# Kernel optimization log

Hardware: AMD Instinct MI355X
Metric: run time of the kernel (lower is better)

## Reference

```python
import jax, jax.numpy as jnp
import numpy as np

N_CLASS = 20          # foreground classes (VOC)
SCORE_THR = 0.05
NMS_THR = 0.3
IMG_H, IMG_W = 600, 800
R = 2000              # number of proposed ROIs


def setup_inputs() -> dict:
    key = jax.random.key(0)
    k1, k2, k3, k4, k5 = jax.random.split(key, 5)
    # well-formed proposal boxes (y1, x1, y2, x2)
    cy = jax.random.uniform(k1, (R,), minval=0.0, maxval=float(IMG_H))
    cx = jax.random.uniform(k2, (R,), minval=0.0, maxval=float(IMG_W))
    hw = jax.random.uniform(k3, (R, 2), minval=20.0, maxval=200.0)
    h, w = hw[:, 0], hw[:, 1]
    boxes = jnp.stack([
        jnp.clip(cy - 0.5 * h, 0.0, IMG_H),
        jnp.clip(cx - 0.5 * w, 0.0, IMG_W),
        jnp.clip(cy + 0.5 * h, 0.0, IMG_H),
        jnp.clip(cx + 0.5 * w, 0.0, IMG_W),
    ], axis=1).astype(jnp.float32)
    loc = (0.2 * jax.random.normal(k4, (R, 4 * (N_CLASS + 1)))).astype(jnp.float32)
    score = (2.0 * jax.random.normal(k5, (R, N_CLASS + 1))).astype(jnp.float32)
    return {
        "proposed_roi_bboxes": boxes,
        "predicted_roi_loc": loc,
        "predicted_roi_score": score,
        "img_height": IMG_H,
        "img_width": IMG_W,
    }


def _pairwise_iou(b):
    # b: [N, 4] in (y1, x1, y2, x2); IoU is invariant to axis order
    tl = jnp.maximum(b[:, None, :2], b[None, :, :2])
    br = jnp.minimum(b[:, None, 2:], b[None, :, 2:])
    wh = jnp.clip(br - tl, 0.0)
    inter = wh[..., 0] * wh[..., 1]
    area = (b[:, 2] - b[:, 0]) * (b[:, 3] - b[:, 1])
    union = area[:, None] + area[None, :] - inter
    return inter / jnp.maximum(union, 1e-9)


def _nms_keep(boxes_sorted, valid_sorted, thr):
    # boxes sorted by descending score; returns keep mask [N]
    N = boxes_sorted.shape[0]
    iou = _pairwise_iou(boxes_sorted)          # [N, N]
    idx = jnp.arange(N)
    def body(suppressed, i):
        keep_i = valid_sorted[i] & (~suppressed[i])
        suppressed = suppressed | (keep_i & (iou[i] > thr) & (idx > i))
        return suppressed, keep_i
    _, keep = jax.lax.scan(body, jnp.zeros((N,), bool), idx)
    return keep


def _detect(proposed_roi_bboxes, predicted_roi_loc, predicted_roi_score, H, W):
    Rn = proposed_roi_bboxes.shape[0]
    C1 = N_CLASS + 1
    b = proposed_roi_bboxes
    loc = predicted_roi_loc.reshape(Rn, C1, 4)
    # Utility.loc2bbox (y1,x1,y2,x2 <-> cy,cx,h,w)
    src_h = b[:, 2] - b[:, 0]
    src_w = b[:, 3] - b[:, 1]
    src_cy = b[:, 0] + 0.5 * src_h
    src_cx = b[:, 1] + 0.5 * src_w
    dy, dx, dh, dw = loc[..., 0], loc[..., 1], loc[..., 2], loc[..., 3]
    cy = dy * src_h[:, None] + src_cy[:, None]
    cx = dx * src_w[:, None] + src_cx[:, None]
    hh = jnp.exp(dh) * src_h[:, None]
    ww = jnp.exp(dw) * src_w[:, None]
    boxes = jnp.stack([cy - 0.5 * hh, cx - 0.5 * ww,
                       cy + 0.5 * hh, cx + 0.5 * ww], axis=-1)  # [R, C1, 4]
    # clamp: even coords (y) to [0,H], odd coords (x) to [0,W]
    boxes = jnp.stack([
        jnp.clip(boxes[..., 0], 0.0, H),
        jnp.clip(boxes[..., 1], 0.0, W),
        jnp.clip(boxes[..., 2], 0.0, H),
        jnp.clip(boxes[..., 3], 0.0, W),
    ], axis=-1)
    prob = jax.nn.softmax(predicted_roi_score, axis=1)          # [R, C1]

    # foreground classes 1..N_CLASS -> leading class axis [C, R, ...]
    fg_boxes = jnp.transpose(boxes[:, 1:, :], (1, 0, 2))        # [C, R, 4]
    fg_prob = prob[:, 1:].T                                     # [C, R]
    valid = fg_prob > SCORE_THR
    sort_key = jnp.where(valid, fg_prob, -jnp.inf)
    order = jnp.argsort(-sort_key, axis=1)                      # [C, R]
    boxes_s = jnp.take_along_axis(fg_boxes, order[..., None], axis=1)
    prob_s = jnp.take_along_axis(fg_prob, order, axis=1)
    valid_s = jnp.take_along_axis(valid, order, axis=1)

    keep = jax.vmap(_nms_keep, in_axes=(0, 0, None))(boxes_s, valid_s, NMS_THR)  # [C, R] bool

    km = keep.astype(boxes_s.dtype)
    out = jnp.concatenate([boxes_s, prob_s[..., None]], axis=-1) * km[..., None]  # [C, R, 5]
    labels = jnp.arange(1, N_CLASS + 1, dtype=boxes_s.dtype)[:, None] * km        # [C, R]
    return out, labels, keep


def reference(proposed_roi_bboxes, predicted_roi_loc, predicted_roi_score,
              img_height, img_width):
    out, labels, keep = _detect(proposed_roi_bboxes, predicted_roi_loc,
                                predicted_roi_score, float(img_height), float(img_width))
    return out, labels, keep
```

## Files before the change

### kernel.cpp

```cpp
#include <hip/hip_runtime.h>
#include <cstdint>

#pragma clang fp contract(off)

#define R_N   2000
#define C1    21
#define NCLS  20
#define MAXFV 512
#define OUT_LBL   200000
#define OUT_KEEP  240000
#define FMARGIN   4.0f

#define WAVE_SYNC() do {                                        \
  __builtin_amdgcn_sched_barrier(0);                            \
  asm volatile("s_waitcnt lgkmcnt(0)" ::: "memory");            \
  __builtin_amdgcn_sched_barrier(0);                            \
} while (0)

__device__ __forceinline__ double read_dim(const void* p) {
  int iv = *(const int*)p;
  if (iv >= 1 && iv <= 1000000) return (double)iv;
  float fv = *(const float*)p;
  if (fv >= 1.0f && fv <= 1000000.0f) return (double)fv;
  return *(const double*)p;
}

__global__ __launch_bounds__(256) void prep3_kernel(
    const float* __restrict__ rois, const float* __restrict__ loc,
    const float* __restrict__ score,
    const void* __restrict__ hptr, const void* __restrict__ wptr,
    double4* __restrict__ dbox_all, double* __restrict__ prob_t,
    float* __restrict__ out)
{
  int tid = blockIdx.x * 256 + threadIdx.x;
  float4 z4 = make_float4(0.f, 0.f, 0.f, 0.f);
  for (int z = tid; z < 70000; z += 168 * 256) ((float4*)out)[z] = z4;

  if (tid < 40000) {
    int r = tid % R_N, c = tid / R_N;
    const double H = read_dim(hptr), W = read_dim(wptr);
    const float* l4 = loc + r * 84 + (c + 1) * 4;
    double dy = (double)l4[0], dx = (double)l4[1];
    double eh = exp((double)l4[2]), ew = exp((double)l4[3]);
    double b0 = (double)rois[r*4+0], b1 = (double)rois[r*4+1];
    double b2 = (double)rois[r*4+2], b3 = (double)rois[r*4+3];
    double sh  = b2 - b0,       sw  = b3 - b1;
    double scy = b0 + 0.5*sh,   scx = b1 + 0.5*sw;
    double cy = dy*sh + scy,    cx = dx*sw + scx;
    double hh = eh*sh,          ww = ew*sw;
    double y1 = fmin(fmax(cy - 0.5*hh, 0.0), H);
    double x1 = fmin(fmax(cx - 0.5*ww, 0.0), W);
    double y2 = fmin(fmax(cy + 0.5*hh, 0.0), H);
    double x2 = fmin(fmax(cx + 0.5*ww, 0.0), W);
    dbox_all[c * R_N + r] = make_double4(y1, x1, y2, x2);
  } else if (tid >= 40960 && tid < 40960 + R_N) {
    int r = tid - 40960;
    const float* sc = score + r * C1;
    double m = (double)sc[0];
    #pragma unroll
    for (int k = 1; k < C1; ++k) m = fmax(m, (double)sc[k]);
    double e[C1]; double s = 0.0;
    #pragma unroll
    for (int k = 0; k < C1; ++k) { e[k] = exp((double)sc[k] - m); s += e[k]; }
    #pragma unroll
    for (int c = 0; c < NCLS; ++c) prob_t[c * R_N + r] = e[c + 1] / s;
  }
}

__global__ __launch_bounds__(256) void sortexport_kernel(
    const float* __restrict__ rois, const float* __restrict__ loc,
    const float* __restrict__ score,
    const void* __restrict__ hptr, const void* __restrict__ wptr,
    float* __restrict__ out,
    const double4* __restrict__ dbox_all, const double* __restrict__ prob_t,
    float4* __restrict__ fbox4, double4* __restrict__ dbox4s,
    float* __restrict__ farea, float* __restrict__ sprobg,
    int* __restrict__ vcls, int mode)
{
  __shared__ double sbd[R_N][4];
  __shared__ ulonglong2 keys[2048];
  __shared__ double klist64[2][64][5];
  __shared__ float  klist32[2][64][5];
  __shared__ int kcnt[2];
  __shared__ int wsum[4];

  const int cls = blockIdx.x;
  const int t = threadIdx.x;
  const int lane = t & 63, wid = t >> 6;

  ulonglong2 rk[8];
  int vmask = 0;
  #pragma unroll
  for (int u = 0; u < 8; ++u) {
    int r = t + 256 * u;
    rk[u] = make_ulonglong2(0ull, 0ull);
    if (r < R_N) {
      double p;
      if (mode) {
        p = prob_t[cls * R_N + r];
      } else {
        const float* sc = score + r * C1;
        double m = (double)sc[0];
        #pragma unroll
        for (int k = 1; k < C1; ++k) m = fmax(m, (double)sc[k]);
        double s = 0.0;
        #pragma unroll
        for (int k = 0; k < C1; ++k) s += exp((double)sc[k] - m);
        p = exp((double)sc[cls + 1] - m) / s;
      }
      if (p > 0.05) {
        rk[u] = make_ulonglong2((unsigned long long)__double_as_longlong(p),
                                (unsigned long long)(unsigned int)(~r));
        vmask |= 1 << u;
      }
    }
  }

  int cnt = __popc(vmask);
  int x = cnt;
  #pragma unroll
  for (int off = 1; off < 64; off <<= 1) {
    int y = __shfl_up(x, off);
    if (lane >= off) x += y;
  }
  if (lane == 63) wsum[wid] = x;
  __syncthreads();
  int woff = 0;
  #pragma unroll
  for (int w2 = 0; w2 < 4; ++w2) { int s = wsum[w2]; if (w2 < wid) woff += s; }
  const int V = wsum[0] + wsum[1] + wsum[2] + wsum[3];
  int pos = woff + x - cnt;
  #pragma unroll
  for (int u = 0; u < 8; ++u)
    if ((vmask >> u) & 1) keys[pos++] = rk[u];

  int NSORT = 64; while (NSORT < V) NSORT <<= 1;
  for (int j = V + t; j < NSORT; j += 256)
    keys[j] = make_ulonglong2(0ull, (unsigned long long)(unsigned int)(~(unsigned)j));
  __syncthreads();

  const int wb = 128 * wid;
  int wsz = NSORT - wb; if (wsz > 128) wsz = 128;
  for (int k = 2; k <= NSORT; k <<= 1) {
    int js = k >> 1;
    if (js >= 128) {
      for (; js >= 128; js >>= 1) {
        __syncthreads();
        for (int p = t; p < (NSORT >> 1); p += 256) {
          int i = ((p & ~(js - 1)) << 1) | (p & (js - 1));
          int j = i | js;
          ulonglong2 a = keys[i], b = keys[j];
          bool altb = (a.x < b.x) || (a.x == b.x && a.y < b.y);
          if (altb == ((i & k) == 0)) { keys[i] = b; keys[j] = a; }
        }
      }
      __syncthreads();
    }
    if (wsz > 0) {
      for (; js > 0; js >>= 1) {
        if (lane < (wsz >> 1)) {
          int i = wb + (((lane & ~(js - 1)) << 1) | (lane & (js - 1)));
          int j = i | js;
          ulonglong2 a = keys[i], b = keys[j];
          bool altb = (a.x < b.x) || (a.x == b.x && a.y < b.y);
          if (altb == ((i & k) == 0)) { keys[i] = b; keys[j] = a; }
        }
        WAVE_SYNC();
      }
    }
  }
  __syncthreads();

  if (mode && V <= MAXFV) {
    for (int j = t; j < V; j += 256) {
      ulonglong2 kj = keys[j];
      int idx = (int)(~(unsigned)kj.y);
      double4 bd = dbox_all[cls * R_N + idx];
      int g = cls * MAXFV + j;
      fbox4[g]  = make_float4((float)bd.x, (float)bd.y, (float)bd.z, (float)bd.w);
      dbox4s[g] = bd;
      farea[g]  = (float)((bd.z - bd.x) * (bd.w - bd.y));
      sprobg[g] = (float)__longlong_as_double((long long)kj.x);
    }
    if (t == 0) vcls[cls] = V;
    return;
  }
  if (mode && t == 0) vcls[cls] = V;

  #pragma unroll
  for (int u = 0; u < 8; ++u) {
    int r = t + 256 * u;
    if (r < R_N) {
      if (mode) {
        double4 bd = dbox_all[cls * R_N + r];
        sbd[r][0]=bd.x; sbd[r][1]=bd.y; sbd[r][2]=bd.z; sbd[r][3]=bd.w;
      } else {
        const double H = read_dim(hptr), W = read_dim(wptr);
        const float* l4 = loc + r * 84 + (cls + 1) * 4;
        double dy = (double)l4[0], dx = (double)l4[1];
        double eh = exp((double)l4[2]), ew = exp((double)l4[3]);
        double b0 = (double)rois[r*4+0], b1 = (double)rois[r*4+1];
        double b2 = (double)rois[r*4+2], b3 = (double)rois[r*4+3];
        double sh  = b2 - b0,       sw  = b3 - b1;
        double scy = b0 + 0.5*sh,   scx = b1 + 0.5*sw;
        double cy = dy*sh + scy,    cx = dx*sw + scx;
        double hh = eh*sh,          ww = ew*sw;
        sbd[r][0] = fmin(fmax(cy - 0.5*hh, 0.0), H);
        sbd[r][1] = fmin(fmax(cx - 0.5*ww, 0.0), W);
        sbd[r][2] = fmin(fmax(cy + 0.5*hh, 0.0), H);
        sbd[r][3] = fmin(fmax(cx + 0.5*ww, 0.0), W);
      }
    }
  }
  __syncthreads();

  int   idx8[8];
  float fx0[8], fx1[8], fx2[8], fx3[8], far5[8], pr[8];
  unsigned am = 0, km = 0;
  #pragma unroll
  for (int q = 0; q < 8; ++q) {
    int j = t + 256 * q;
    fx0[q]=fx1[q]=fx2[q]=fx3[q]=far5[q]=pr[q]=0.f; idx8[q]=0;
    if (j < V) {
      int idx = (int)(~(unsigned)keys[j].y);
      idx8[q] = idx;
      double a0=sbd[idx][0], a1=sbd[idx][1], a2=sbd[idx][2], a3=sbd[idx][3];
      fx0[q]=(float)a0; fx1[q]=(float)a1; fx2[q]=(float)a2; fx3[q]=(float)a3;
      far5[q]=(float)((a2-a0)*(a3-a1));
      pr[q]=(float)__longlong_as_double((long long)keys[j].x);
      am |= 1u << q;
    }
  }

  #pragma unroll
  for (int q = 0; q < 8; ++q) {
    if (256 * q >= V) break;
    for (int sub = 0; sub < 4; ++sub) {
      const int ch = 4 * q + sub;
      if (64 * ch >= V) break;
      const int buf = ch & 1;
      if (wid == sub) {
        const int s = 64 * ch + lane;
        bool a = ((am >> q) & 1u) != 0u;
        int myidx = idx8[q];
        float f0=fx0[q], f1=fx1[q], f2=fx2[q], f3=fx3[q], fa=far5[q];
        unsigned long long m = __ballot(a);
        unsigned long long kept = 0;
        while (m) {
          int i = __ffsll(m) - 1;
          m &= m - 1;
          kept |= 1ull << i;
          float k0=__shfl(f0,i), k1=__shfl(f1,i), k2=__shfl(f2,i), k3=__shfl(f3,i), ka=__shfl(fa,i);
          bool aliveL = ((m >> lane) & 1ull) != 0ull;
          float ty=fmaxf(k0,f0), tx=fmaxf(k1,f1);
          float by=fminf(k2,f2), bz=fminf(k3,f3);
          float w0=fmaxf(by-ty,0.f), w1=fmaxf(bz-tx,0.f);
          float inter=w0*w1;
          float uni=fmaxf(ka+fa-inter, 1e-9f);
          float rhs=0.3f*uni;
          bool kill = aliveL && (inter > rhs + FMARGIN);
          bool amb  = aliveL && !kill && (inter > rhs - FMARGIN);
          if (__any(amb)) {
            int kidx = __shfl(myidx, i);
            double b0=sbd[kidx][0], b1=sbd[kidx][1], b2=sbd[kidx][2], b3=sbd[kidx][3];
            double bar=(b2-b0)*(b3-b1);
            if (amb) {
              double a0=sbd[myidx][0], a1=sbd[myidx][1], a2=sbd[myidx][2], a3=sbd[myidx][3];
              double aar=(a2-a0)*(a3-a1);
              double ty_=fmax(b0,a0), tx_=fmax(b1,a1);
              double by_=fmin(b2,a2), bz_=fmin(b3,a3);
              double w0_=fmax(by_-ty_,0.0), w1_=fmax(bz_-tx_,0.0);
              double in_=w0_*w1_;
              double un_=bar+aar-in_;
              if (in_/fmax(un_,1e-9) > 0.3) kill = true;
            }
          }
          m &= ~__ballot(kill);
        }
        am &= ~(1u << q);
        if ((kept >> lane) & 1ull) {
          km |= 1u << q;
          int kpos = (int)__popcll(kept & ((1ull << lane) - 1ull));
          double a0=sbd[myidx][0], a1=sbd[myidx][1], a2=sbd[myidx][2], a3=sbd[myidx][3];
          klist64[buf][kpos][0]=a0; klist64[buf][kpos][1]=a1;
          klist64[buf][kpos][2]=a2; klist64[buf][kpos][3]=a3;
          klist64[buf][kpos][4]=(a2-a0)*(a3-a1);
          klist32[buf][kpos][0]=f0; klist32[buf][kpos][1]=f1;
          klist32[buf][kpos][2]=f2; klist32[buf][kpos][3]=f3; klist32[buf][kpos][4]=fa;
        }
        if (lane == 0) kcnt[buf] = (int)__popcll(kept);
      }
      __syncthreads();
      const int nk = kcnt[buf];
      const int jmin = 64 * (ch + 1);
      for (int n = 0; n < nk; ++n) {
        float k0=klist32[buf][n][0], k1=klist32[buf][n][1];
        float k2=klist32[buf][n][2], k3=klist32[buf][n][3], ka=klist32[buf][n][4];
        #pragma unroll
        for (int q2 = 0; q2 < 8; ++q2) {
          if (256 * q2 >= V) break;
          int j2 = t + 256 * q2;
          if (((am >> q2) & 1u) && j2 >= jmin) {
            float ty=fmaxf(k0,fx0[q2]), tx=fmaxf(k1,fx1[q2]);
            float by=fminf(k2,fx2[q2]), bz=fminf(k3,fx3[q2]);
            float w0=fmaxf(by-ty,0.f), w1=fmaxf(bz-tx,0.f);
            float inter=w0*w1;
            float uni=fmaxf(ka+far5[q2]-inter, 1e-9f);
            float rhs=0.3f*uni;
            if (inter > rhs + FMARGIN) {
              am &= ~(1u << q2);
            } else if (inter > rhs - FMARGIN) {
              int idx = idx8[q2];
              double a0=sbd[idx][0], a1=sbd[idx][1], a2=sbd[idx][2], a3=sbd[idx][3];
              double ar_=(a2-a0)*(a3-a1);
              double b0=klist64[buf][n][0], b1=klist64[buf][n][1];
              double b2=klist64[buf][n][2], b3=klist64[buf][n][3], br=klist64[buf][n][4];
              double ty_=fmax(b0,a0), tx_=fmax(b1,a1);
              double by_=fmin(b2,a2), bz_=fmin(b3,a3);
              double w0_=fmax(by_-ty_,0.0), w1_=fmax(bz_-tx_,0.0);
              double in_=w0_*w1_;
              double un_=br+ar_-in_;
              if (in_/fmax(un_,1e-9) > 0.3) am &= ~(1u << q2);
            }
          }
        }
      }
    }
  }

  #pragma unroll
  for (int u = 0; u < 8; ++u) {
    int j = t + 256 * u;
    if (j < R_N) {
      int row = cls * R_N + j;
      bool k = ((km >> u) & 1u) != 0u;
      out[row*5+0] = k ? fx0[u] : 0.f;
      out[row*5+1] = k ? fx1[u] : 0.f;
      out[row*5+2] = k ? fx2[u] : 0.f;
      out[row*5+3] = k ? fx3[u] : 0.f;
      out[row*5+4] = k ? pr[u]  : 0.f;
      out[OUT_LBL  + row] = k ? (float)(cls + 1) : 0.f;
      out[OUT_KEEP + row] = k ? 1.f : 0.f;
    }
  }
}

__global__ __launch_bounds__(256) void build_kernel(
    const float4* __restrict__ fbox4, const float* __restrict__ farea,
    const double4* __restrict__ dbox4s, const int* __restrict__ vcls,
    unsigned long long* __restrict__ kw)
{
  const int cls = blockIdx.x;
  const int V = vcls[cls];
  if (V > MAXFV) return;
  int n = blockIdx.y * 256 + threadIdx.x;
  int c = 0;
  #pragma unroll
  for (int cc = 1; cc < 8; ++cc) if (n >= 32*cc*(cc+1)) c = cc;
  int rem = n - 32*c*(c+1);
  int jq = rem / (c + 1);
  int j = 64*c + jq;
  int w = rem - jq*(c+1);
  if (j >= V) return;

  const float4* fb = fbox4 + cls * MAXFV;
  const float*  fa = farea + cls * MAXFV;
  float4 mb = fb[j];
  float  ma = fa[j];
  int i0 = 64*w;
  int i1 = min(i0 + 64, j);
  unsigned long long acc = 0ull;
  #pragma unroll 8
  for (int i = i0; i < i1; ++i) {
    float4 bb = fb[i]; float ba = fa[i];
    float ty=fmaxf(bb.x,mb.x), tx=fmaxf(bb.y,mb.y);
    float by=fminf(bb.z,mb.z), bz=fminf(bb.w,mb.w);
    float w0=fmaxf(by-ty,0.f), w1=fmaxf(bz-tx,0.f);
    float inter=w0*w1;
    float uni=fmaxf(ba+ma-inter, 1e-9f);
    float rhs=0.3f*uni;
    bool kill = inter > rhs + FMARGIN;
    if (!kill && inter > rhs - FMARGIN) {
      double4 bd = dbox4s[cls*MAXFV + i];
      double4 md = dbox4s[cls*MAXFV + j];
      double bar=(bd.z-bd.x)*(bd.w-bd.y);
      double dar=(md.z-md.x)*(md.w-md.y);
      double ty_=fmax(bd.x,md.x), tx_=fmax(bd.y,md.y);
      double by_=fmin(bd.z,md.z), bz_=fmin(bd.w,md.w);
      double w0_=fmax(by_-ty_,0.0), w1_=fmax(bz_-tx_,0.0);
      double in_=w0_*w1_;
      double un_=bar+dar-in_;
      kill = in_/fmax(un_,1e-9) > 0.3;
    }
    acc |= (unsigned long long)(kill ? 1 : 0) << (i & 63);
  }
  kw[(size_t)(cls*MAXFV + j)*8 + w] = acc;
}

__global__ __launch_bounds__(256) void scan_kernel(
    float* __restrict__ out,
    const float4* __restrict__ fbox4, const float* __restrict__ sprobg,
    const unsigned long long* __restrict__ kw, const int* __restrict__ vcls)
{
  __shared__ unsigned long long ckill[2][8][256];
  __shared__ unsigned long long keptm[8];
  const int cls = blockIdx.x;
  const int V = vcls[cls];
  if (V > MAXFV) return;
  const int t = threadIdx.x, lane = t & 63, wid = t >> 6;

  unsigned long long ckq[2] = {0ull, 0ull};
  unsigned am = 0;
  #pragma unroll
  for (int q = 0; q < 2; ++q) {
    int j = t + 256*q;
    if (j < V) {
      am |= 1u << q;
      const unsigned long long* src = kw + (size_t)(cls*MAXFV + j)*8;
      int c = wid + 4*q;
      for (int w = 0; w < c; ++w) ckill[q][w][t] = src[w];
      ckq[q] = src[c];
    }
  }

  unsigned km = 0;
  #pragma unroll
  for (int q = 0; q < 2; ++q) {
    if (256*q >= V) break;
    for (int sub = 0; sub < 4; ++sub) {
      const int ch = 4*q + sub;
      if (64*ch >= V) break;
      if (wid == sub) {
        bool a = ((am >> q) & 1u) != 0u;
        unsigned long long m = __ballot(a);
        unsigned long long kept = 0ull;
        while (m) {
          int i = __ffsll(m) - 1;
          unsigned long long bit = 1ull << i;
          kept |= bit; m &= ~bit;
          bool kill = ((ckq[q] >> i) & 1ull) != 0ull;
          m &= ~__ballot(kill);
        }
        am &= ~(1u << q);
        if ((kept >> lane) & 1ull) km |= 1u << q;
        if (lane == 0) keptm[ch] = kept;
      }
      __syncthreads();
      unsigned long long K = keptm[ch];
      #pragma unroll
      for (int q2 = 0; q2 < 2; ++q2) {
        if (256*q2 >= V) break;
        if (((am >> q2) & 1u) && (wid + 4*q2) > ch) {
          if (ckill[q2][ch][t] & K) am &= ~(1u << q2);
        }
      }
    }
  }

  #pragma unroll
  for (int q = 0; q < 2; ++q) {
    int j = t + 256*q;
    if (j < V && ((km >> q) & 1u)) {
      int row = cls*R_N + j;
      float4 b = fbox4[cls*MAXFV + j];
      out[row*5+0]=b.x; out[row*5+1]=b.y; out[row*5+2]=b.z; out[row*5+3]=b.w;
      out[row*5+4]=sprobg[cls*MAXFV + j];
      out[OUT_LBL  + row] = (float)(cls + 1);
      out[OUT_KEEP + row] = 1.f;
    }
  }
}

extern "C" void kernel_launch(void* const* d_in, const int* in_sizes, int n_in,
                              void* d_out, int out_size, void* d_ws, size_t ws_size,
                              hipStream_t stream) {
  const float* rois  = (const float*)d_in[0];
  const float* loc   = (const float*)d_in[1];
  const float* score = (const float*)d_in[2];
  const void*  hp    = d_in[3];
  const void*  wp    = d_in[4];
  float* out = (float*)d_out;

  char* wsb = (char*)d_ws;
  double4* dbox_all = (double4*)(wsb + 0);
  double*  prob_t   = (double*)(wsb + 1280000);
  float4*  fbox4    = (float4*)(wsb + 1600000);
  double4* dbox4s   = (double4*)(wsb + 1763840);
  float*   farea    = (float*)(wsb + 2091520);
  float*   sprob    = (float*)(wsb + 2132480);
  unsigned long long* kw = (unsigned long long*)(wsb + 2173440);
  int*     vcls     = (int*)(wsb + 2828800);
  const size_t WS_NEED = 2828880;

  if (ws_size >= WS_NEED) {
    prep3_kernel<<<dim3(168), dim3(256), 0, stream>>>(rois, loc, score, hp, wp,
                                                      dbox_all, prob_t, out);
    sortexport_kernel<<<dim3(NCLS), dim3(256), 0, stream>>>(
        rois, loc, score, hp, wp, out, dbox_all, prob_t,
        fbox4, dbox4s, farea, sprob, vcls, 1);
    build_kernel<<<dim3(NCLS, 9), dim3(256), 0, stream>>>(fbox4, farea, dbox4s, vcls, kw);
    scan_kernel<<<dim3(NCLS), dim3(256), 0, stream>>>(out, fbox4, sprob, kw, vcls);
  } else {
    sortexport_kernel<<<dim3(NCLS), dim3(256), 0, stream>>>(
        rois, loc, score, hp, wp, out, (const double4*)nullptr, (const double*)nullptr,
        (float4*)nullptr, (double4*)nullptr, (float*)nullptr, (float*)nullptr,
        (int*)nullptr, 0);
  }
}
```

Before: 52.55 us.

## Fuse sort, mask-build and scan kernels into one persistent kernel with flag sync

Merges the sort/export, IoU kill-mask build and greedy scan kernels into a single launch of a 20x10 grid. Worker blocks (y>0) spin on a per-class ready flag, compute the kill bitmasks and bump a done counter. Leader blocks (y==0) sort, publish their data, wait for all 9 workers and then run the scan reusing shared memory. This removes two kernel launch boundaries but depends on all 200 blocks being co-resident to avoid deadlock, and adds spin-wait latency. The fallback path gets a standalone sortexport kernel.

Measured after the change: 81.74 us. 1.56x slower.

```diff
diff --git a/kernel.cpp b/kernel.cpp
--- a/kernel.cpp
+++ b/kernel.cpp
@@ -30,7 +30,7 @@
     const float* __restrict__ score,
     const void* __restrict__ hptr, const void* __restrict__ wptr,
     double4* __restrict__ dbox_all, double* __restrict__ prob_t,
-    float* __restrict__ out)
+    float* __restrict__ out, int* __restrict__ flags)
 {
   int tid = blockIdx.x * 256 + threadIdx.x;
   float4 z4 = make_float4(0.f, 0.f, 0.f, 0.f);
@@ -64,29 +64,88 @@
     for (int k = 0; k < C1; ++k) { e[k] = exp((double)sc[k] - m); s += e[k]; }
     #pragma unroll
     for (int c = 0; c < NCLS; ++c) prob_t[c * R_N + r] = e[c + 1] / s;
+  } else if (tid >= 42960 && tid < 43000) {
+    flags[tid - 42960] = 0;
   }
 }
 
-__global__ __launch_bounds__(256) void sortexport_kernel(
-    const float* __restrict__ rois, const float* __restrict__ loc,
-    const float* __restrict__ score,
-    const void* __restrict__ hptr, const void* __restrict__ wptr,
+__global__ __launch_bounds__(256) void nmspipe_kernel(
     float* __restrict__ out,
     const double4* __restrict__ dbox_all, const double* __restrict__ prob_t,
     float4* __restrict__ fbox4, double4* __restrict__ dbox4s,
     float* __restrict__ farea, float* __restrict__ sprobg,
-    int* __restrict__ vcls, int mode)
+    int* __restrict__ vcls, unsigned long long* __restrict__ kw,
+    int* __restrict__ ready, int* __restrict__ done)
 {
   __shared__ double sbd[R_N][4];
   __shared__ ulonglong2 keys[2048];
   __shared__ double klist64[2][64][5];
   __shared__ float  klist32[2][64][5];
+  __shared__ unsigned long long keptm[8];
   __shared__ int kcnt[2];
   __shared__ int wsum[4];
 
   const int cls = blockIdx.x;
   const int t = threadIdx.x;
   const int lane = t & 63, wid = t >> 6;
+
+  if (blockIdx.y != 0) {
+    if (t == 0) {
+      while (__hip_atomic_load(&ready[cls], __ATOMIC_ACQUIRE,
+                               __HIP_MEMORY_SCOPE_AGENT) == 0)
+        __builtin_amdgcn_s_sleep(8);
+    }
+    __syncthreads();
+    const int V = vcls[cls];
+    if (V <= MAXFV) {
+      int n = (blockIdx.y - 1) * 256 + t;
+      int c = 0;
+      #pragma unroll
+      for (int cc = 1; cc < 8; ++cc) if (n >= 32*cc*(cc+1)) c = cc;
+      int rem = n - 32*c*(c+1);
+      int jq = rem / (c + 1);
+      int j = 64*c + jq;
+      int w = rem - jq*(c+1);
+      if (j < V) {
+        const float4* fb = fbox4 + cls * MAXFV;
+        const float*  fa = farea + cls * MAXFV;
+        float4 mb = fb[j];
+        float  ma = fa[j];
+        int i0 = 64*w;
+        int i1 = min(i0 + 64, j);
+        unsigned long long acc = 0ull;
+        #pragma unroll 8
+        for (int i = i0; i < i1; ++i) {
+          float4 bb = fb[i]; float ba = fa[i];
+          float ty=fmaxf(bb.x,mb.x), tx=fmaxf(bb.y,mb.y);
+          float by=fminf(bb.z,mb.z), bz=fminf(bb.w,mb.w);
+          float w0=fmaxf(by-ty,0.f), w1=fmaxf(bz-tx,0.f);
+          float inter=w0*w1;
+          float uni=fmaxf(ba+ma-inter, 1e-9f);
+          float rhs=0.3f*uni;
+          bool kill = inter > rhs + FMARGIN;
+          if (!kill && inter > rhs - FMARGIN) {
+            double4 bd = dbox4s[cls*MAXFV + i];
+            double4 md = dbox4s[cls*MAXFV + j];
+            double bar=(bd.z-bd.x)*(bd.w-bd.y);
+            double dar=(md.z-md.x)*(md.w-md.y);
+            double ty_=fmax(bd.x,md.x), tx_=fmax(bd.y,md.y);
+            double by_=fmin(bd.z,md.z), bz_=fmin(bd.w,md.w);
+            double w0_=fmax(by_-ty_,0.0), w1_=fmax(bz_-tx_,0.0);
+            double in_=w0_*w1_;
+            double un_=bar+dar-in_;
+            kill = in_/fmax(un_,1e-9) > 0.3;
+          }
+          acc |= (unsigned long long)(kill ? 1 : 0) << (i & 63);
+        }
+        kw[(size_t)(cls*MAXFV + j)*8 + w] = acc;
+      }
+    }
+    __syncthreads();
+    __threadfence();
+    if (t == 0) atomicAdd(&done[cls], 1);
+    return;
+  }
 
   ulonglong2 rk[8];
   int vmask = 0;
@@ -95,19 +154,7 @@
     int r = t + 256 * u;
     rk[u] = make_ulonglong2(0ull, 0ull);
     if (r < R_N) {
-      double p;
-      if (mode) {
-        p = prob_t[cls * R_N + r];
-      } else {
-        const float* sc = score + r * C1;
-        double m = (double)sc[0];
-        #pragma unroll
-        for (int k = 1; k < C1; ++k) m = fmax(m, (double)sc[k]);
-        double s = 0.0;
-        #pragma unroll
-        for (int k = 0; k < C1; ++k) s += exp((double)sc[k] - m);
-        p = exp((double)sc[cls + 1] - m) / s;
-      }
+      double p = prob_t[cls * R_N + r];
       if (p > 0.05) {
         rk[u] = make_ulonglong2((unsigned long long)__double_as_longlong(p),
                                 (unsigned long long)(unsigned int)(~r));
@@ -171,7 +218,7 @@
   }
   __syncthreads();
 
-  if (mode && V <= MAXFV) {
+  if (V <= MAXFV) {
     for (int j = t; j < V; j += 256) {
       ulonglong2 kj = keys[j];
       int idx = (int)(~(unsigned)kj.y);
@@ -182,34 +229,94 @@
       farea[g]  = (float)((bd.z - bd.x) * (bd.w - bd.y));
       sprobg[g] = (float)__longlong_as_double((long long)kj.x);
     }
-    if (t == 0) vcls[cls] = V;
+    __syncthreads();
+    __threadfence();
+    if (t == 0) {
+      vcls[cls] = V;
+      __threadfence();
+      __hip_atomic_store(&ready[cls], 1, __ATOMIC_RELEASE, __HIP_MEMORY_SCOPE_AGENT);
+      while (__hip_atomic_load(&done[cls], __ATOMIC_ACQUIRE,
+                               __HIP_MEMORY_SCOPE_AGENT) < 9)
+        __builtin_amdgcn_s_sleep(8);
+    }
+    __syncthreads();
+
+    unsigned long long (*ckill)[8][256] = (unsigned long long (*)[8][256])keys;
+    unsigned long long ckq[2] = {0ull, 0ull};
+    unsigned am = 0;
+    #pragma unroll
+    for (int q = 0; q < 2; ++q) {
+      int j = t + 256*q;
+      if (j < V) {
+        am |= 1u << q;
+        const unsigned long long* src = kw + (size_t)(cls*MAXFV + j)*8;
+        int c = wid + 4*q;
+        for (int w = 0; w < c; ++w) ckill[q][w][t] = src[w];
+        ckq[q] = src[c];
+      }
+    }
+    __syncthreads();
+
+    unsigned km = 0;
+    #pragma unroll
+    for (int q = 0; q < 2; ++q) {
+      if (256*q >= V) break;
+      for (int sub = 0; sub < 4; ++sub) {
+        const int ch = 4*q + sub;
+        if (64*ch >= V) break;
+        if (wid == sub) {
+          bool a = ((am >> q) & 1u) != 0u;
+          unsigned long long m = __ballot(a);
+          unsigned long long kept = 0ull;
+          while (m) {
+            int i = __ffsll(m) - 1;
+            unsigned long long bit = 1ull << i;
+            kept |= bit; m &= ~bit;
+            bool kill = ((ckq[q] >> i) & 1ull) != 0ull;
+            m &= ~__ballot(kill);
+          }
+          am &= ~(1u << q);
+          if ((kept >> lane) & 1ull) km |= 1u << q;
+          if (lane == 0) keptm[ch] = kept;
+        }
+        __syncthreads();
+        unsigned long long K = keptm[ch];
+        #pragma unroll
+        for (int q2 = 0; q2 < 2; ++q2) {
+          if (256*q2 >= V) break;
+          if (((am >> q2) & 1u) && (wid + 4*q2) > ch) {
+            if (ckill[q2][ch][t] & K) am &= ~(1u << q2);
+          }
+        }
+      }
+    }
+
+    #pragma unroll
+    for (int q = 0; q < 2; ++q) {
+      int j = t + 256*q;
+      if (j < V && ((km >> q) & 1u)) {
+        int row = cls*R_N + j;
+        float4 b = fbox4[cls*MAXFV + j];
+        out[row*5+0]=b.x; out[row*5+1]=b.y; out[row*5+2]=b.z; out[row*5+3]=b.w;
+        out[row*5+4]=sprobg[cls*MAXFV + j];
+        out[OUT_LBL  + row] = (float)(cls + 1);
+        out[OUT_KEEP + row] = 1.f;
+      }
+    }
     return;
   }
-  if (mode && t == 0) vcls[cls] = V;
-
+
+  if (t == 0) {
+    vcls[cls] = V;
+    __threadfence();
+    __hip_atomic_store(&ready[cls], 1, __ATOMIC_RELEASE, __HIP_MEMORY_SCOPE_AGENT);
+  }
   #pragma unroll
   for (int u = 0; u < 8; ++u) {
     int r = t + 256 * u;
     if (r < R_N) {
-      if (mode) {
-        double4 bd = dbox_all[cls * R_N + r];
-        sbd[r][0]=bd.x; sbd[r][1]=bd.y; sbd[r][2]=bd.z; sbd[r][3]=bd.w;
-      } else {
-        const double H = read_dim(hptr), W = read_dim(wptr);
-        const float* l4 = loc + r * 84 + (cls + 1) * 4;
-        double dy = (double)l4[0], dx = (double)l4[1];
-        double eh = exp((double)l4[2]), ew = exp((double)l4[3]);
-        double b0 = (double)rois[r*4+0], b1 = (double)rois[r*4+1];
-        double b2 = (double)rois[r*4+2], b3 = (double)rois[r*4+3];
-        double sh  = b2 - b0,       sw  = b3 - b1;
-        double scy = b0 + 0.5*sh,   scx = b1 + 0.5*sw;
-        double cy = dy*sh + scy,    cx = dx*sw + scx;
-        double hh = eh*sh,          ww = ew*sw;
-        sbd[r][0] = fmin(fmax(cy - 0.5*hh, 0.0), H);
-        sbd[r][1] = fmin(fmax(cx - 0.5*ww, 0.0), W);
-        sbd[r][2] = fmin(fmax(cy + 0.5*hh, 0.0), H);
-        sbd[r][3] = fmin(fmax(cx + 0.5*ww, 0.0), W);
-      }
+      double4 bd = dbox_all[cls * R_N + r];
+      sbd[r][0]=bd.x; sbd[r][1]=bd.y; sbd[r][2]=bd.z; sbd[r][3]=bd.w;
     }
   }
   __syncthreads();
@@ -240,7 +347,6 @@
       if (64 * ch >= V) break;
       const int buf = ch & 1;
       if (wid == sub) {
-        const int s = 64 * ch + lane;
         bool a = ((am >> q) & 1u) != 0u;
         int myidx = idx8[q];
         float f0=fx0[q], f1=fx1[q], f2=fx2[q], f3=fx3[q], fa=far5[q];
@@ -345,128 +451,222 @@
   }
 }
 
-__global__ __launch_bounds__(256) void build_kernel(
-    const float4* __restrict__ fbox4, const float* __restrict__ farea,
-    const double4* __restrict__ dbox4s, const int* __restrict__ vcls,
-    unsigned long long* __restrict__ kw)
+__global__ __launch_bounds__(256) void sortexport_kernel(
+    const float* __restrict__ rois, const float* __restrict__ loc,
+    const float* __restrict__ score,
+    const void* __restrict__ hptr, const void* __restrict__ wptr,
+    float* __restrict__ out)
 {
+  __shared__ double sbd[R_N][4];
+  __shared__ ulonglong2 keys[2048];
+  __shared__ double klist64[2][64][5];
+  __shared__ float  klist32[2][64][5];
+  __shared__ int kcnt[2];
+  __shared__ int wsum[4];
+
   const int cls = blockIdx.x;
-  const int V = vcls[cls];
-  if (V > MAXFV) return;
-  int n = blockIdx.y * 256 + threadIdx.x;
-  int c = 0;
-  #pragma unroll
-  for (int cc = 1; cc < 8; ++cc) if (n >= 32*cc*(cc+1)) c = cc;
-  int rem = n - 32*c*(c+1);
-  int jq = rem / (c + 1);
-  int j = 64*c + jq;
-  int w = rem - jq*(c+1);
-  if (j >= V) return;
-
-  const float4* fb = fbox4 + cls * MAXFV;
-  const float*  fa = farea + cls * MAXFV;
-  float4 mb = fb[j];
-  float  ma = fa[j];
-  int i0 = 64*w;
-  int i1 = min(i0 + 64, j);
-  unsigned long long acc = 0ull;
-  #pragma unroll 8
-  for (int i = i0; i < i1; ++i) {
-    float4 bb = fb[i]; float ba = fa[i];
-    float ty=fmaxf(bb.x,mb.x), tx=fmaxf(bb.y,mb.y);
-    float by=fminf(bb.z,mb.z), bz=fminf(bb.w,mb.w);
-    float w0=fmaxf(by-ty,0.f), w1=fmaxf(bz-tx,0.f);
-    float inter=w0*w1;
-    float uni=fmaxf(ba+ma-inter, 1e-9f);
-    float rhs=0.3f*uni;
-    bool kill = inter > rhs + FMARGIN;
-    if (!kill && inter > rhs - FMARGIN) {
-      double4 bd = dbox4s[cls*MAXFV + i];
-      double4 md = dbox4s[cls*MAXFV + j];
-      double bar=(bd.z-bd.x)*(bd.w-bd.y);
-      double dar=(md.z-md.x)*(md.w-md.y);
-      double ty_=fmax(bd.x,md.x), tx_=fmax(bd.y,md.y);
-      double by_=fmin(bd.z,md.z), bz_=fmin(bd.w,md.w);
-      double w0_=fmax(by_-ty_,0.0), w1_=fmax(bz_-tx_,0.0);
-      double in_=w0_*w1_;
-      double un_=bar+dar-in_;
-      kill = in_/fmax(un_,1e-9) > 0.3;
-    }
-    acc |= (unsigned long long)(kill ? 1 : 0) << (i & 63);
-  }
-  kw[(size_t)(cls*MAXFV + j)*8 + w] = acc;
-}
-
-__global__ __launch_bounds__(256) void scan_kernel(
-    float* __restrict__ out,
-    const float4* __restrict__ fbox4, const float* __restrict__ sprobg,
-    const unsigned long long* __restrict__ kw, const int* __restrict__ vcls)
-{
-  __shared__ unsigned long long ckill[2][8][256];
-  __shared__ unsigned long long keptm[8];
-  const int cls = blockIdx.x;
-  const int V = vcls[cls];
-  if (V > MAXFV) return;
-  const int t = threadIdx.x, lane = t & 63, wid = t >> 6;
-
-  unsigned long long ckq[2] = {0ull, 0ull};
-  unsigned am = 0;
-  #pragma unroll
-  for (int q = 0; q < 2; ++q) {
-    int j = t + 256*q;
+  const int t = threadIdx.x;
+  const int lane = t & 63, wid = t >> 6;
+  const double H = read_dim(hptr), W = read_dim(wptr);
+
+  ulonglong2 rk[8];
+  int vmask = 0;
+  #pragma unroll
+  for (int u = 0; u < 8; ++u) {
+    int r = t + 256 * u;
+    rk[u] = make_ulonglong2(0ull, 0ull);
+    if (r < R_N) {
+      const float* sc = score + r * C1;
+      double m = (double)sc[0];
+      #pragma unroll
+      for (int k = 1; k < C1; ++k) m = fmax(m, (double)sc[k]);
+      double s = 0.0;
+      #pragma unroll
+      for (int k = 0; k < C1; ++k) s += exp((double)sc[k] - m);
+      double p = exp((double)sc[cls + 1] - m) / s;
+      const float* l4 = loc + r * 84 + (cls + 1) * 4;
+      double dy = (double)l4[0], dx = (double)l4[1];
+      double eh = exp((double)l4[2]), ew = exp((double)l4[3]);
+      double b0 = (double)rois[r*4+0], b1 = (double)rois[r*4+1];
+      double b2 = (double)rois[r*4+2], b3 = (double)rois[r*4+3];
+      double sh  = b2 - b0,       sw  = b3 - b1;
+      double scy = b0 + 0.5*sh,   scx = b1 + 0.5*sw;
+      double cy = dy*sh + scy,    cx = dx*sw + scx;
+      double hh = eh*sh,          ww = ew*sw;
+      sbd[r][0] = fmin(fmax(cy - 0.5*hh, 0.0), H);
+      sbd[r][1] = fmin(fmax(cx - 0.5*ww, 0.0), W);
+      sbd[r][2] = fmin(fmax(cy + 0.5*hh, 0.0), H);
+      sbd[r][3] = fmin(fmax(cx + 0.5*ww, 0.0), W);
+      if (p > 0.05) {
+        rk[u] = make_ulonglong2((unsigned long long)__double_as_longlong(p),
+                                (unsigned long long)(unsigned int)(~r));
+        vmask |= 1 << u;
+      }
+    }
+  }
+
+  int cnt = __popc(vmask);
+  int x = cnt;
+  #pragma unroll
+  for (int off = 1; off < 64; off <<= 1) {
+    int y = __shfl_up(x, off);
+    if (lane >= off) x += y;
+  }
+  if (lane == 63) wsum[wid] = x;
+  __syncthreads();
+  int woff = 0;
+  #pragma unroll
+  for (int w2 = 0; w2 < 4; ++w2) { int s = wsum[w2]; if (w2 < wid) woff += s; }
+  const int V = wsum[0] + wsum[1] + wsum[2] + wsum[3];
+  int pos = woff + x - cnt;
+  #pragma unroll
+  for (int u = 0; u < 8; ++u)
+    if ((vmask >> u) & 1) keys[pos++] = rk[u];
+
+  int NSORT = 64; while (NSORT < V) NSORT <<= 1;
+  for (int j = V + t; j < NSORT; j += 256)
+    keys[j] = make_ulonglong2(0ull, (unsigned long long)(unsigned int)(~(unsigned)j));
+  __syncthreads();
+
+  for (int k = 2; k <= NSORT; k <<= 1) {
+    for (int js = k >> 1; js > 0; js >>= 1) {
+      for (int p = t; p < (NSORT >> 1); p += 256) {
+        int i = ((p & ~(js - 1)) << 1) | (p & (js - 1));
+        int j = i | js;
+        ulonglong2 a = keys[i], b = keys[j];
+        bool altb = (a.x < b.x) || (a.x == b.x && a.y < b.y);
+        if (altb == ((i & k) == 0)) { keys[i] = b; keys[j] = a; }
+      }
+      __syncthreads();
+    }
+  }
+
+  int   idx8[8];
+  float fx0[8], fx1[8], fx2[8], fx3[8], far5[8], pr[8];
+  unsigned am = 0, km = 0;
+  #pragma unroll
+  for (int q = 0; q < 8; ++q) {
+    int j = t + 256 * q;
+    fx0[q]=fx1[q]=fx2[q]=fx3[q]=far5[q]=pr[q]=0.f; idx8[q]=0;
     if (j < V) {
+      int idx = (int)(~(unsigned)keys[j].y);
+      idx8[q] = idx;
+      double a0=sbd[idx][0], a1=sbd[idx][1], a2=sbd[idx][2], a3=sbd[idx][3];
+      fx0[q]=(float)a0; fx1[q]=(float)a1; fx2[q]=(float)a2; fx3[q]=(float)a3;
+      far5[q]=(float)((a2-a0)*(a3-a1));
+      pr[q]=(float)__longlong_as_double((long long)keys[j].x);
       am |= 1u << q;
-      const unsigned long long* src = kw + (size_t)(cls*MAXFV + j)*8;
-      int c = wid + 4*q;
-      for (int w = 0; w < c; ++w) ckill[q][w][t] = src[w];
-      ckq[q] = src[c];
-    }
-  }
-
-  unsigned km = 0;
-  #pragma unroll
-  for (int q = 0; q < 2; ++q) {
-    if (256*q >= V) break;
+    }
+  }
+
+  #pragma unroll
+  for (int q = 0; q < 8; ++q) {
+    if (256 * q >= V) break;
     for (int sub = 0; sub < 4; ++sub) {
-      const int ch = 4*q + sub;
-      if (64*ch >= V) break;
+      const int ch = 4 * q + sub;
+      if (64 * ch >= V) break;
+      const int buf = ch & 1;
       if (wid == sub) {
         bool a = ((am >> q) & 1u) != 0u;
+        int myidx = idx8[q];
+        float f0=fx0[q], f1=fx1[q], f2=fx2[q], f3=fx3[q], fa=far5[q];
         unsigned long long m = __ballot(a);
-        unsigned long long kept = 0ull;
+        unsigned long long kept = 0;
         while (m) {
           int i = __ffsll(m) - 1;
-          unsigned long long bit = 1ull << i;
-          kept |= bit; m &= ~bit;
-          bool kill = ((ckq[q] >> i) & 1ull) != 0ull;
+          m &= m - 1;
+          kept |= 1ull << i;
+          float k0=__shfl(f0,i), k1=__shfl(f1,i), k2=__shfl(f2,i), k3=__shfl(f3,i), ka=__shfl(fa,i);
+          bool aliveL = ((m >> lane) & 1ull) != 0ull;
+          float ty=fmaxf(k0,f0), tx=fmaxf(k1,f1);
+          float by=fminf(k2,f2), bz=fminf(k3,f3);
+          float w0=fmaxf(by-ty,0.f), w1=fmaxf(bz-tx,0.f);
+          float inter=w0*w1;
+          float uni=fmaxf(ka+fa-inter, 1e-9f);
+          float rhs=0.3f*uni;
+          bool kill = aliveL && (inter > rhs + FMARGIN);
+          bool amb  = aliveL && !kill && (inter > rhs - FMARGIN);
+          if (__any(amb)) {
+            int kidx = __shfl(myidx, i);
+            double b0=sbd[kidx][0], b1=sbd[kidx][1], b2=sbd[kidx][2], b3=sbd[kidx][3];
+            double bar=(b2-b0)*(b3-b1);
+            if (amb) {
+              double a0=sbd[myidx][0], a1=sbd[myidx][1], a2=sbd[myidx][2], a3=sbd[myidx][3];
+              double aar=(a2-a0)*(a3-a1);
+              double ty_=fmax(b0,a0), tx_=fmax(b1,a1);
+              double by_=fmin(b2,a2), bz_=fmin(b3,a3);
+              double w0_=fmax(by_-ty_,0.0), w1_=fmax(bz_-tx_,0.0);
+              double in_=w0_*w1_;
+              double un_=bar+aar-in_;
+              if (in_/fmax(un_,1e-9) > 0.3) kill = true;
+            }
+          }
           m &= ~__ballot(kill);
         }
         am &= ~(1u << q);
-        if ((kept >> lane) & 1ull) km |= 1u << q;
-        if (lane == 0) keptm[ch] = kept;
+        if ((kept >> lane) & 1ull) {
+          km |= 1u << q;
+          int kpos = (int)__popcll(kept & ((1ull << lane) - 1ull));
+          double a0=sbd[myidx][0], a1=sbd[myidx][1], a2=sbd[myidx][2], a3=sbd[myidx][3];
+          klist64[buf][kpos][0]=a0; klist64[buf][kpos][1]=a1;
+          klist64[buf][kpos][2]=a2; klist64[buf][kpos][3]=a3;
+          klist64[buf][kpos][4]=(a2-a0)*(a3-a1);
+          klist32[buf][kpos][0]=f0; klist32[buf][kpos][1]=f1;
+          klist32[buf][kpos][2]=f2; klist32[buf][kpos][3]=f3; klist32[buf][kpos][4]=fa;
+        }
+        if (lane == 0) kcnt[buf] = (int)__popcll(kept);
       }
       __syncthreads();
-      unsigned long long K = keptm[ch];
-      #pragma unroll
-      for (int q2 = 0; q2 < 2; ++q2) {
-        if (256*q2 >= V) break;
-        if (((am >> q2) & 1u) && (wid + 4*q2) > ch) {
-          if (ckill[q2][ch][t] & K) am &= ~(1u << q2);
-        }
-      }
-    }
-  }
-
-  #pragma unroll
-  for (int q = 0; q < 2; ++q) {
-    int j = t + 256*q;
-    if (j < V && ((km >> q) & 1u)) {
-      int row = cls*R_N + j;
-      float4 b = fbox4[cls*MAXFV + j];
-      out[row*5+0]=b.x; out[row*5+1]=b.y; out[row*5+2]=b.z; out[row*5+3]=b.w;
-      out[row*5+4]=sprobg[cls*MAXFV + j];
-      out[OUT_LBL  + row] = (float)(cls + 1);
-      out[OUT_KEEP + row] = 1.f;
+      const int nk = kcnt[buf];
+      const int jmin = 64 * (ch + 1);
+      for (int n = 0; n < nk; ++n) {
+        float k0=klist32[buf][n][0], k1=klist32[buf][n][1];
+        float k2=klist32[buf][n][2], k3=klist32[buf][n][3], ka=klist32[buf][n][4];
+        #pragma unroll
+        for (int q2 = 0; q2 < 8; ++q2) {
+          if (256 * q2 >= V) break;
+          int j2 = t + 256 * q2;
+          if (((am >> q2) & 1u) && j2 >= jmin) {
+            float ty=fmaxf(k0,fx0[q2]), tx=fmaxf(k1,fx1[q2]);
+            float by=fminf(k2,fx2[q2]), bz=fminf(k3,fx3[q2]);
+            float w0=fmaxf(by-ty,0.f), w1=fmaxf(bz-tx,0.f);
+            float inter=w0*w1;
+            float uni=fmaxf(ka+far5[q2]-inter, 1e-9f);
+            float rhs=0.3f*uni;
+            if (inter > rhs + FMARGIN) {
+              am &= ~(1u << q2);
+            } else if (inter > rhs - FMARGIN) {
+              int idx = idx8[q2];
+              double a0=sbd[idx][0], a1=sbd[idx][1], a2=sbd[idx][2], a3=sbd[idx][3];
+              double ar_=(a2-a0)*(a3-a1);
+              double b0=klist64[buf][n][0], b1=klist64[buf][n][1];
+              double b2=klist64[buf][n][2], b3=klist64[buf][n][3], br=klist64[buf][n][4];
+              double ty_=fmax(b0,a0), tx_=fmax(b1,a1);
+              double by_=fmin(b2,a2), bz_=fmin(b3,a3);
+              double w0_=fmax(by_-ty_,0.0), w1_=fmax(bz_-tx_,0.0);
+              double in_=w0_*w1_;
+              double un_=br+ar_-in_;
+              if (in_/fmax(un_,1e-9) > 0.3) am &= ~(1u << q2);
+            }
+          }
+        }
+      }
+    }
+  }
+
+  #pragma unroll
+  for (int u = 0; u < 8; ++u) {
+    int j = t + 256 * u;
+    if (j < R_N) {
+      int row = cls * R_N + j;
+      bool k = ((km >> u) & 1u) != 0u;
+      out[row*5+0] = k ? fx0[u] : 0.f;
+      out[row*5+1] = k ? fx1[u] : 0.f;
+      out[row*5+2] = k ? fx2[u] : 0.f;
+      out[row*5+3] = k ? fx3[u] : 0.f;
+      out[row*5+4] = k ? pr[u]  : 0.f;
+      out[OUT_LBL  + row] = k ? (float)(cls + 1) : 0.f;
+      out[OUT_KEEP + row] = k ? 1.f : 0.f;
     }
   }
 }
@@ -490,20 +690,18 @@
   float*   sprob    = (float*)(wsb + 2132480);
   unsigned long long* kw = (unsigned long long*)(wsb + 2173440);
   int*     vcls     = (int*)(wsb + 2828800);
-  const size_t WS_NEED = 2828880;
+  int*     flags    = (int*)(wsb + 2828880);
+  int*     ready    = flags;
+  int*     done     = flags + 20;
+  const size_t WS_NEED = 2829040;
 
   if (ws_size >= WS_NEED) {
     prep3_kernel<<<dim3(168), dim3(256), 0, stream>>>(rois, loc, score, hp, wp,
-                                                      dbox_all, prob_t, out);
-    sortexport_kernel<<<dim3(NCLS), dim3(256), 0, stream>>>(
-        rois, loc, score, hp, wp, out, dbox_all, prob_t,
-        fbox4, dbox4s, farea, sprob, vcls, 1);
-    build_kernel<<<dim3(NCLS, 9), dim3(256), 0, stream>>>(fbox4, farea, dbox4s, vcls, kw);
-    scan_kernel<<<dim3(NCLS), dim3(256), 0, stream>>>(out, fbox4, sprob, kw, vcls);
+                                                      dbox_all, prob_t, out, flags);
+    nmspipe_kernel<<<dim3(NCLS, 10), dim3(256), 0, stream>>>(
+        out, dbox_all, prob_t, fbox4, dbox4s, farea, sprob, vcls, kw, ready, done);
   } else {
     sortexport_kernel<<<dim3(NCLS), dim3(256), 0, stream>>>(
-        rois, loc, score, hp, wp, out, (const double4*)nullptr, (const double*)nullptr,
-        (float4*)nullptr, (double4*)nullptr, (float*)nullptr, (float*)nullptr,
-        (int*)nullptr, 0);
+        rois, loc, score, hp, wp, out);
   }
 }
```
